# Performance work log

Measured on AMD Instinct MI355X. Metric: run time of the kernel, lower is better.

## Reference

```python
import jax, jax.numpy as jnp
import numpy as np

EPS = 1e-8

def setup_inputs() -> dict:
    key = jax.random.key(0)
    k1, k2, k3, k4, k5 = jax.random.split(key, 5)
    B, S, d, H = 4, 1024, 512, 8
    hd = d // H
    x = jax.random.normal(k1, (B, S, d), dtype=jnp.float32)
    V = jax.random.normal(k2, (B, S, H, hd), dtype=jnp.float32)
    # binary biological mask [B, S, S]
    M = (jax.random.uniform(k3, (B, S, S)) > 0.5).astype(jnp.float32)
    in_proj_w = jax.random.normal(k4, (3 * d, d), dtype=jnp.float32) * 0.02
    in_proj_b = jnp.zeros((3 * d,), dtype=jnp.float32)
    out_w = jax.random.normal(k5, (d, d), dtype=jnp.float32) * 0.02
    out_b = jnp.zeros((d,), dtype=jnp.float32)
    return {"x": x, "V": V, "M": M, "in_proj_w": in_proj_w,
            "in_proj_b": in_proj_b, "out_w": out_w, "out_b": out_b}


def reference(x, V, M, in_proj_w, in_proj_b, out_w, out_b):
    B, S, d = x.shape
    H, hd = V.shape[2], V.shape[3]
    # packed QKV projection (torch MHA in_proj); V slice is computed by torch
    # but its result is discarded, so only Q,K slices influence the output.
    qkv = x @ in_proj_w.T + in_proj_b            # [B, S, 3d]
    q = qkv[..., :d].reshape(B, S, H, hd).transpose(0, 2, 1, 3)        # [B,H,S,hd]
    k = qkv[..., d:2 * d].reshape(B, S, H, hd).transpose(0, 2, 1, 3)   # [B,H,S,hd]
    scores = jnp.einsum("bhqd,bhkd->bhqk", q, k) / jnp.sqrt(jnp.float32(hd))
    A = jax.nn.softmax(scores, axis=-1)           # [B,H,S,S] per-head attn weights
    # biological mask + L1 renormalization (post-hoc, as in original)
    A_sparse = A * M[:, None, :, :]
    norm = jnp.sum(jnp.abs(A_sparse), axis=-1, keepdims=True) + EPS
    A_bar = A_sparse / norm
    # custom V: [B,S,H,hd] -> [B,H,S,hd]
    Vp = V.transpose(0, 2, 1, 3)
    out = jnp.einsum("bhqk,bhkd->bhqd", A_bar, Vp)  # [B,H,S,hd]
    out = out.transpose(0, 2, 1, 3).reshape(B, S, d)
    return out @ out_w.T + out_b
```

## Files before the change

kernel.cpp:

```cpp
#include <hip/hip_runtime.h>
#include <hip/hip_bf16.h>

#define BB 4
#define SS 1024
#define DD 512
#define HH 8
#define HD 64

typedef __attribute__((ext_vector_type(8))) short bf16x8;
typedef __attribute__((ext_vector_type(4))) float f32x4;

static __device__ __forceinline__ unsigned short f2b(float f) {
  union { float f; unsigned int u; } c; c.f = f;
  return (unsigned short)((c.u + 0x7fffu + ((c.u >> 16) & 1u)) >> 16);
}

__global__ __launch_bounds__(256) void prep(
    const float* __restrict__ x, const float* __restrict__ W1,
    const float* __restrict__ Wo, const float* __restrict__ Mmask,
    const float* __restrict__ V, unsigned short* __restrict__ xb,
    unsigned short* __restrict__ W1b, unsigned short* __restrict__ Wob,
    unsigned char* __restrict__ Mpack, unsigned short* __restrict__ Vt) {
  __shared__ float Ls[64][65];
  const int bid = blockIdx.x;
  const int tid = threadIdx.x;

  if (bid < 1408) {
    const float* src; unsigned short* dst; size_t off;
    if (bid < 1024) { src = x;  dst = xb;  off = ((size_t)bid * 256 + tid) * 8; }
    else if (bid < 1280) { src = W1; dst = W1b; off = ((size_t)(bid - 1024) * 256 + tid) * 8; }
    else { src = Wo; dst = Wob; off = ((size_t)(bid - 1280) * 256 + tid) * 8; }
    const float4 a = *(const float4*)(src + off);
    const float4 b = *(const float4*)(src + off + 4);
    union { unsigned short s[8]; uint4 v; } o;
    o.s[0] = f2b(a.x); o.s[1] = f2b(a.y); o.s[2] = f2b(a.z); o.s[3] = f2b(a.w);
    o.s[4] = f2b(b.x); o.s[5] = f2b(b.y); o.s[6] = f2b(b.z); o.s[7] = f2b(b.w);
    *(uint4*)(dst + off) = o.v;
  } else if (bid < 3456) {
    const size_t g = (size_t)(bid - 1408) * 256 + tid;
    const float4 a = *(const float4*)(Mmask + g * 8);
    const float4 b = *(const float4*)(Mmask + g * 8 + 4);
    unsigned v = 0;
    v |= (a.x > 0.5f) ? 1u : 0u;   v |= (a.y > 0.5f) ? 2u : 0u;
    v |= (a.z > 0.5f) ? 4u : 0u;   v |= (a.w > 0.5f) ? 8u : 0u;
    v |= (b.x > 0.5f) ? 16u : 0u;  v |= (b.y > 0.5f) ? 32u : 0u;
    v |= (b.z > 0.5f) ? 64u : 0u;  v |= (b.w > 0.5f) ? 128u : 0u;
    Mpack[g] = (unsigned char)v;
  } else {
    const int id = bid - 3456;
    const int s0 = (id & 15) * 64, h = (id >> 4) & 7, b = id >> 7;
    {
      const int r = tid >> 2, cs = (tid & 3) * 16;
      const float* src = V + ((size_t)((b * SS + s0 + r) * HH) + h) * HD + cs;
#pragma unroll
      for (int j = 0; j < 4; j++) {
        const float4 v = *(const float4*)(src + j * 4);
        Ls[r][cs + j * 4 + 0] = v.x; Ls[r][cs + j * 4 + 1] = v.y;
        Ls[r][cs + j * 4 + 2] = v.z; Ls[r][cs + j * 4 + 3] = v.w;
      }
    }
    __syncthreads();
    {
      const int d = tid >> 2, ss = (tid & 3) * 16;
      union { unsigned short s[16]; uint4 v[2]; } o;
#pragma unroll
      for (int j = 0; j < 16; j++) o.s[j] = f2b(Ls[ss + j][d]);
      unsigned short* dst =
          Vt + ((size_t)((b * HH + h) * HD + d)) * SS + s0 + ss;
      *(uint4*)dst = o.v[0];
      *(uint4*)(dst + 8) = o.v[1];
    }
  }
}

__global__ __launch_bounds__(256) void gemm_qk(
    const unsigned short* __restrict__ xb, const unsigned short* __restrict__ W1b,
    const float* __restrict__ bias, unsigned short* __restrict__ qkb) {
  __shared__ unsigned short As[128][40];
  __shared__ unsigned short Bs[64][40];
  const int tid = threadIdx.x;
  const int lane = tid & 63, wave = tid >> 6;
  const int l16 = lane & 15, quad = lane >> 4;
  const int row0 = blockIdx.y * 128, col0 = blockIdx.x * 64;

  f32x4 acc[2][4];
#pragma unroll
  for (int i = 0; i < 2; i++)
#pragma unroll
    for (int j = 0; j < 4; j++) acc[i][j] = (f32x4){0.f, 0.f, 0.f, 0.f};

  for (int k0 = 0; k0 < DD; k0 += 32) {
    __syncthreads();
    {
      const int r = tid >> 1, cs = (tid & 1) * 16;
      const unsigned short* s = xb + (size_t)(row0 + r) * DD + k0 + cs;
      *(uint4*)&As[r][cs] = *(const uint4*)s;
      *(uint4*)&As[r][cs + 8] = *(const uint4*)(s + 8);
    }
    {
      const int r = tid >> 2, cs = (tid & 3) * 8;
      *(uint4*)&Bs[r][cs] =
          *(const uint4*)(W1b + (size_t)(col0 + r) * DD + k0 + cs);
    }
    __syncthreads();

    const bf16x8 a0 = *(const bf16x8*)&As[wave * 32 + l16][quad * 8];
    const bf16x8 a1 = *(const bf16x8*)&As[wave * 32 + 16 + l16][quad * 8];
#pragma unroll
    for (int nt = 0; nt < 4; nt++) {
      const bf16x8 bb = *(const bf16x8*)&Bs[nt * 16 + l16][quad * 8];
      acc[0][nt] = __builtin_amdgcn_mfma_f32_16x16x32_bf16(a0, bb, acc[0][nt], 0, 0, 0);
      acc[1][nt] = __builtin_amdgcn_mfma_f32_16x16x32_bf16(a1, bb, acc[1][nt], 0, 0, 0);
    }
  }

#pragma unroll
  for (int nt = 0; nt < 4; nt++) {
    const int col = col0 + nt * 16 + l16;
    const float bv = bias[col];
#pragma unroll
    for (int mi = 0; mi < 2; mi++)
#pragma unroll
      for (int reg = 0; reg < 4; reg++) {
        const int row = row0 + wave * 32 + mi * 16 + quad * 4 + reg;
        qkb[(size_t)row * 1024 + col] = f2b(acc[mi][nt][reg] + bv);
      }
  }
}

__global__ __launch_bounds__(256) void gemm_out(
    const unsigned short* __restrict__ Ab, const unsigned short* __restrict__ Wob,
    const float* __restrict__ bias, float* __restrict__ out) {
  __shared__ unsigned short As[64][40];
  __shared__ unsigned short Bs[64][40];
  const int tid = threadIdx.x;
  const int lane = tid & 63, wave = tid >> 6;
  const int l16 = lane & 15, quad = lane >> 4;
  const int row0 = blockIdx.y * 64, col0 = blockIdx.x * 64;

  f32x4 acc[4];
#pragma unroll
  for (int j = 0; j < 4; j++) acc[j] = (f32x4){0.f, 0.f, 0.f, 0.f};

  for (int k0 = 0; k0 < DD; k0 += 32) {
    __syncthreads();
    {
      const int r = tid >> 2, cs = (tid & 3) * 8;
      *(uint4*)&As[r][cs] =
          *(const uint4*)(Ab + (size_t)(row0 + r) * DD + k0 + cs);
      *(uint4*)&Bs[r][cs] =
          *(const uint4*)(Wob + (size_t)(col0 + r) * DD + k0 + cs);
    }
    __syncthreads();

    const bf16x8 a0 = *(const bf16x8*)&As[wave * 16 + l16][quad * 8];
#pragma unroll
    for (int nt = 0; nt < 4; nt++) {
      const bf16x8 bb = *(const bf16x8*)&Bs[nt * 16 + l16][quad * 8];
      acc[nt] = __builtin_amdgcn_mfma_f32_16x16x32_bf16(a0, bb, acc[nt], 0, 0, 0);
    }
  }

#pragma unroll
  for (int nt = 0; nt < 4; nt++) {
    const int col = col0 + nt * 16 + l16;
    const float bv = bias[col];
#pragma unroll
    for (int reg = 0; reg < 4; reg++) {
      const int row = row0 + wave * 16 + quad * 4 + reg;
      out[(size_t)row * DD + col] = acc[nt][reg] + bv;
    }
  }
}

__global__ __launch_bounds__(256) void flash_attn_split(
    const unsigned short* __restrict__ qkb, const unsigned short* __restrict__ Vt,
    const unsigned char* __restrict__ Mpack, float* __restrict__ Opart,
    float* __restrict__ Sms) {
  __shared__ unsigned short QP[64][72];
  __shared__ unsigned short Ks[64][72];
  __shared__ unsigned short Vs[64][72];

  const int tid = threadIdx.x;
  const int lane = tid & 63, wave = tid >> 6;
  const int l16 = lane & 15, quad = lane >> 4;
  const int q0 = blockIdx.x * 64;
  const int h = blockIdx.y & 7, sp = blockIdx.y >> 3;
  const int b = blockIdx.z;

  {
    const int r = tid >> 2, cs = (tid & 3) * 16;
    const unsigned short* s = qkb + (size_t)(b * SS + q0 + r) * 1024 + h * HD + cs;
    *(uint4*)&QP[r][cs] = *(const uint4*)s;
    *(uint4*)&QP[r][cs + 8] = *(const uint4*)(s + 8);
  }

  union { uint4 v[4]; unsigned w[16]; } mu;
  {
    const uint4* mp = (const uint4*)(Mpack +
        (size_t)(b * SS + q0 + wave * 16 + l16) * 128 + sp * 64);
    mu.v[0] = mp[0]; mu.v[1] = mp[1]; mu.v[2] = mp[2]; mu.v[3] = mp[3];
  }

  __syncthreads();
  const bf16x8 bQ0 = *(const bf16x8*)&QP[wave * 16 + l16][quad * 8];
  const bf16x8 bQ1 = *(const bf16x8*)&QP[wave * 16 + l16][32 + quad * 8];
  unsigned short(*Ps)[72] = (unsigned short(*)[72]) & QP[wave * 16][0];

  float Smp = 0.f;
  f32x4 O[4];
#pragma unroll
  for (int i = 0; i < 4; i++) O[i] = (f32x4){0.f, 0.f, 0.f, 0.f};

#pragma unroll
  for (int i = 0; i < 8; i++) {
    const int k0 = (sp * 8 + i) * 64;
    const unsigned mlo = mu.w[2 * i], mhi = mu.w[2 * i + 1];

    __syncthreads();
    {
      const int r = tid >> 2, cs = (tid & 3) * 16;
      const unsigned short* s =
          qkb + (size_t)(b * SS + k0 + r) * 1024 + DD + h * HD + cs;
      *(uint4*)&Ks[r][cs] = *(const uint4*)s;
      *(uint4*)&Ks[r][cs + 8] = *(const uint4*)(s + 8);
    }
    {
      const int d = tid >> 2, cs = (tid & 3) * 16;
      const unsigned short* s =
          Vt + ((size_t)((b * HH + h) * HD + d)) * SS + k0 + cs;
      *(uint4*)&Vs[d][cs] = *(const uint4*)s;
      *(uint4*)&Vs[d][cs + 8] = *(const uint4*)(s + 8);
    }
    __syncthreads();

#pragma unroll
    for (int t = 0; t < 4; t++) {
      const bf16x8 aK0 = *(const bf16x8*)&Ks[t * 16 + l16][quad * 8];
      const bf16x8 aK1 = *(const bf16x8*)&Ks[t * 16 + l16][32 + quad * 8];
      f32x4 a = (f32x4){0.f, 0.f, 0.f, 0.f};
      a = __builtin_amdgcn_mfma_f32_16x16x32_bf16(aK0, bQ0, a, 0, 0, 0);
      a = __builtin_amdgcn_mfma_f32_16x16x32_bf16(aK1, bQ1, a, 0, 0, 0);
      const unsigned nib =
          ((t < 2 ? mlo : mhi) >> ((t & 1) * 16 + quad * 4)) & 0xFu;
      float e0 = __expf(a[0] * 0.125f); e0 = (nib & 1u) ? e0 : 0.f;
      float e1 = __expf(a[1] * 0.125f); e1 = (nib & 2u) ? e1 : 0.f;
      float e2 = __expf(a[2] * 0.125f); e2 = (nib & 4u) ? e2 : 0.f;
      float e3 = __expf(a[3] * 0.125f); e3 = (nib & 8u) ? e3 : 0.f;
      Smp += (e0 + e1) + (e2 + e3);
      uint2 w;
      w.x = (unsigned)f2b(e0) | ((unsigned)f2b(e1) << 16);
      w.y = (unsigned)f2b(e2) | ((unsigned)f2b(e3) << 16);
      *(uint2*)&Ps[l16][t * 16 + quad * 4] = w;
    }

    const bf16x8 aP0 = *(const bf16x8*)&Ps[l16][quad * 8];
    const bf16x8 aP1 = *(const bf16x8*)&Ps[l16][32 + quad * 8];
#pragma unroll
    for (int dt = 0; dt < 4; dt++) {
      const bf16x8 bV0 = *(const bf16x8*)&Vs[dt * 16 + l16][quad * 8];
      const bf16x8 bV1 = *(const bf16x8*)&Vs[dt * 16 + l16][32 + quad * 8];
      O[dt] = __builtin_amdgcn_mfma_f32_16x16x32_bf16(aP0, bV0, O[dt], 0, 0, 0);
      O[dt] = __builtin_amdgcn_mfma_f32_16x16x32_bf16(aP1, bV1, O[dt], 0, 0, 0);
    }
  }

  Smp += __shfl_xor(Smp, 16);
  Smp += __shfl_xor(Smp, 32);
  const size_t grow0 = (size_t)(b * HH + h) * SS + q0 + wave * 16;
  const int NR = BB * HH * SS;
  if (lane < 16) Sms[(size_t)sp * NR + grow0 + lane] = Smp;
#pragma unroll
  for (int reg = 0; reg < 4; reg++) {
    const size_t obase = ((size_t)sp * NR + grow0 + quad * 4 + reg) * HD;
#pragma unroll
    for (int dt = 0; dt < 4; dt++)
      Opart[obase + dt * 16 + l16] = O[dt][reg];
  }
}

__global__ __launch_bounds__(256) void combine(
    const float* __restrict__ Opart, const float* __restrict__ Sms,
    unsigned short* __restrict__ attnb) {
  const int idx = blockIdx.x * 256 + threadIdx.x;
  const int row = idx >> 4;
  const int d = (idx & 15) * 4;
  const int NR = BB * HH * SS;
  const float4 o0 = *(const float4*)(Opart + (size_t)row * HD + d);
  const float4 o1 = *(const float4*)(Opart + ((size_t)NR + row) * HD + d);
  const float s = Sms[row] + Sms[NR + row];
  const float inv = 1.0f / (s + 1e-12f);
  const int b = row >> 13, h = (row >> 10) & 7, q = row & 1023;
  union { unsigned short us[4]; uint2 v; } o;
  o.us[0] = f2b((o0.x + o1.x) * inv);
  o.us[1] = f2b((o0.y + o1.y) * inv);
  o.us[2] = f2b((o0.z + o1.z) * inv);
  o.us[3] = f2b((o0.w + o1.w) * inv);
  *(uint2*)(attnb + (size_t)(b * SS + q) * DD + h * HD + d) = o.v;
}

extern "C" void kernel_launch(void* const* d_in, const int* in_sizes, int n_in,
                              void* d_out, int out_size, void* d_ws,
                              size_t ws_size, hipStream_t stream) {
  const float* x = (const float*)d_in[0];
  const float* V = (const float*)d_in[1];
  const float* Mmask = (const float*)d_in[2];
  const float* in_proj_w = (const float*)d_in[3];
  const float* in_proj_b = (const float*)d_in[4];
  const float* out_w = (const float*)d_in[5];
  const float* out_b = (const float*)d_in[6];
  float* out = (float*)d_out;

  unsigned char* ws = (unsigned char*)d_ws;
  unsigned short* qkb   = (unsigned short*)(ws);
  unsigned short* xb    = (unsigned short*)(ws + (8ull << 20));
  unsigned short* W1b   = (unsigned short*)(ws + (12ull << 20));
  unsigned short* Wob   = (unsigned short*)(ws + (13ull << 20));
  unsigned short* Vt    = (unsigned short*)(ws + (14ull << 20));
  unsigned short* attnb = (unsigned short*)(ws + (18ull << 20));
  float*          Opart = (float*)(ws + (22ull << 20));
  float*          Sms   = (float*)(ws + (38ull << 20));
  unsigned char*  Mpack = ws + (38ull << 20) + (256u << 10);

  prep<<<3968, 256, 0, stream>>>(x, in_proj_w, out_w, Mmask, V,
                                 xb, W1b, Wob, Mpack, Vt);
  gemm_qk<<<dim3(16, 32), 256, 0, stream>>>(xb, W1b, in_proj_b, qkb);
  flash_attn_split<<<dim3(SS / 64, 2 * HH, BB), 256, 0, stream>>>(
      qkb, Vt, Mpack, Opart, Sms);
  combine<<<2048, 256, 0, stream>>>(Opart, Sms, attnb);
  gemm_out<<<dim3(8, 64), 256, 0, stream>>>(attnb, Wob, out_b, out);
}
```

Measured before the change: 144.2 us.

## Fuse split-K attention combine into a 512-thread attention block via LDS reduction

The attention kernel now runs both key halves inside one 512-thread block. Waves 4-7 handle the second half of the keys and pass their partial outputs and row sums through shared memory, so the block writes normalized bf16 output directly. This removes the separate combine kernel and the fp32 partial-output round trip through global memory. Separately, the QK projection GEMM tile shrinks from 128 to 64 rows, doubling its grid. The larger block and added shared memory may lower attention occupancy, and the smaller GEMM tile reduces reuse of the loaded weight tile.

```diff
diff --git a/kernel.cpp b/kernel.cpp
--- a/kernel.cpp
+++ b/kernel.cpp
@@ -76,41 +76,33 @@
 __global__ __launch_bounds__(256) void gemm_qk(
     const unsigned short* __restrict__ xb, const unsigned short* __restrict__ W1b,
     const float* __restrict__ bias, unsigned short* __restrict__ qkb) {
-  __shared__ unsigned short As[128][40];
+  __shared__ unsigned short As[64][40];
   __shared__ unsigned short Bs[64][40];
   const int tid = threadIdx.x;
   const int lane = tid & 63, wave = tid >> 6;
   const int l16 = lane & 15, quad = lane >> 4;
-  const int row0 = blockIdx.y * 128, col0 = blockIdx.x * 64;
-
-  f32x4 acc[2][4];
-#pragma unroll
-  for (int i = 0; i < 2; i++)
-#pragma unroll
-    for (int j = 0; j < 4; j++) acc[i][j] = (f32x4){0.f, 0.f, 0.f, 0.f};
+  const int row0 = blockIdx.y * 64, col0 = blockIdx.x * 64;
+
+  f32x4 acc[4];
+#pragma unroll
+  for (int j = 0; j < 4; j++) acc[j] = (f32x4){0.f, 0.f, 0.f, 0.f};
 
   for (int k0 = 0; k0 < DD; k0 += 32) {
     __syncthreads();
     {
-      const int r = tid >> 1, cs = (tid & 1) * 16;
-      const unsigned short* s = xb + (size_t)(row0 + r) * DD + k0 + cs;
-      *(uint4*)&As[r][cs] = *(const uint4*)s;
-      *(uint4*)&As[r][cs + 8] = *(const uint4*)(s + 8);
-    }
-    {
       const int r = tid >> 2, cs = (tid & 3) * 8;
+      *(uint4*)&As[r][cs] =
+          *(const uint4*)(xb + (size_t)(row0 + r) * DD + k0 + cs);
       *(uint4*)&Bs[r][cs] =
           *(const uint4*)(W1b + (size_t)(col0 + r) * DD + k0 + cs);
     }
     __syncthreads();
 
-    const bf16x8 a0 = *(const bf16x8*)&As[wave * 32 + l16][quad * 8];
-    const bf16x8 a1 = *(const bf16x8*)&As[wave * 32 + 16 + l16][quad * 8];
+    const bf16x8 a0 = *(const bf16x8*)&As[wave * 16 + l16][quad * 8];
 #pragma unroll
     for (int nt = 0; nt < 4; nt++) {
       const bf16x8 bb = *(const bf16x8*)&Bs[nt * 16 + l16][quad * 8];
-      acc[0][nt] = __builtin_amdgcn_mfma_f32_16x16x32_bf16(a0, bb, acc[0][nt], 0, 0, 0);
-      acc[1][nt] = __builtin_amdgcn_mfma_f32_16x16x32_bf16(a1, bb, acc[1][nt], 0, 0, 0);
+      acc[nt] = __builtin_amdgcn_mfma_f32_16x16x32_bf16(a0, bb, acc[nt], 0, 0, 0);
     }
   }
 
@@ -119,12 +111,10 @@
     const int col = col0 + nt * 16 + l16;
     const float bv = bias[col];
 #pragma unroll
-    for (int mi = 0; mi < 2; mi++)
-#pragma unroll
-      for (int reg = 0; reg < 4; reg++) {
-        const int row = row0 + wave * 32 + mi * 16 + quad * 4 + reg;
-        qkb[(size_t)row * 1024 + col] = f2b(acc[mi][nt][reg] + bv);
-      }
+    for (int reg = 0; reg < 4; reg++) {
+      const int row = row0 + wave * 16 + quad * 4 + reg;
+      qkb[(size_t)row * 1024 + col] = f2b(acc[nt][reg] + bv);
+    }
   }
 }
 
@@ -173,71 +163,69 @@
   }
 }
 
-__global__ __launch_bounds__(256) void flash_attn_split(
+__global__ __launch_bounds__(512) void flash_attn(
     const unsigned short* __restrict__ qkb, const unsigned short* __restrict__ Vt,
-    const unsigned char* __restrict__ Mpack, float* __restrict__ Opart,
-    float* __restrict__ Sms) {
-  __shared__ unsigned short QP[64][72];
-  __shared__ unsigned short Ks[64][72];
-  __shared__ unsigned short Vs[64][72];
+    const unsigned char* __restrict__ Mpack, unsigned short* __restrict__ attnb) {
+  __shared__ unsigned short Qs[64][72];
+  __shared__ unsigned short Ks[2][64][72];
+  __shared__ unsigned short Vs[2][64][72];
+  __shared__ unsigned short Ps[8][16][72];
 
   const int tid = threadIdx.x;
   const int lane = tid & 63, wave = tid >> 6;
   const int l16 = lane & 15, quad = lane >> 4;
+  const int qg = wave & 3, kh = wave >> 2;
   const int q0 = blockIdx.x * 64;
-  const int h = blockIdx.y & 7, sp = blockIdx.y >> 3;
+  const int h = blockIdx.y;
   const int b = blockIdx.z;
 
   {
-    const int r = tid >> 2, cs = (tid & 3) * 16;
-    const unsigned short* s = qkb + (size_t)(b * SS + q0 + r) * 1024 + h * HD + cs;
-    *(uint4*)&QP[r][cs] = *(const uint4*)s;
-    *(uint4*)&QP[r][cs + 8] = *(const uint4*)(s + 8);
+    const int r = tid >> 3, cs = (tid & 7) * 8;
+    *(uint4*)&Qs[r][cs] =
+        *(const uint4*)(qkb + (size_t)(b * SS + q0 + r) * 1024 + h * HD + cs);
   }
 
   union { uint4 v[4]; unsigned w[16]; } mu;
   {
     const uint4* mp = (const uint4*)(Mpack +
-        (size_t)(b * SS + q0 + wave * 16 + l16) * 128 + sp * 64);
+        (size_t)(b * SS + q0 + qg * 16 + l16) * 128 + kh * 64);
     mu.v[0] = mp[0]; mu.v[1] = mp[1]; mu.v[2] = mp[2]; mu.v[3] = mp[3];
   }
 
   __syncthreads();
-  const bf16x8 bQ0 = *(const bf16x8*)&QP[wave * 16 + l16][quad * 8];
-  const bf16x8 bQ1 = *(const bf16x8*)&QP[wave * 16 + l16][32 + quad * 8];
-  unsigned short(*Ps)[72] = (unsigned short(*)[72]) & QP[wave * 16][0];
+  const bf16x8 bQ0 = *(const bf16x8*)&Qs[qg * 16 + l16][quad * 8];
+  const bf16x8 bQ1 = *(const bf16x8*)&Qs[qg * 16 + l16][32 + quad * 8];
 
   float Smp = 0.f;
   f32x4 O[4];
 #pragma unroll
   for (int i = 0; i < 4; i++) O[i] = (f32x4){0.f, 0.f, 0.f, 0.f};
 
-#pragma unroll
+  const unsigned short* kbase = qkb + (size_t)(b * SS) * 1024 + DD + h * HD;
+  const unsigned short* vbase = Vt + (size_t)((b * HH + h) * HD) * SS;
+
+#pragma unroll 2
   for (int i = 0; i < 8; i++) {
-    const int k0 = (sp * 8 + i) * 64;
     const unsigned mlo = mu.w[2 * i], mhi = mu.w[2 * i + 1];
 
     __syncthreads();
     {
-      const int r = tid >> 2, cs = (tid & 3) * 16;
-      const unsigned short* s =
-          qkb + (size_t)(b * SS + k0 + r) * 1024 + DD + h * HD + cs;
-      *(uint4*)&Ks[r][cs] = *(const uint4*)s;
-      *(uint4*)&Ks[r][cs + 8] = *(const uint4*)(s + 8);
-    }
-    {
-      const int d = tid >> 2, cs = (tid & 3) * 16;
-      const unsigned short* s =
-          Vt + ((size_t)((b * HH + h) * HD + d)) * SS + k0 + cs;
-      *(uint4*)&Vs[d][cs] = *(const uint4*)s;
-      *(uint4*)&Vs[d][cs + 8] = *(const uint4*)(s + 8);
+      const int r = tid >> 3, cs = (tid & 7) * 8;
+      *(uint4*)&Ks[0][r][cs] =
+          *(const uint4*)(kbase + (size_t)(i * 64 + r) * 1024 + cs);
+      *(uint4*)&Ks[1][r][cs] =
+          *(const uint4*)(kbase + (size_t)(512 + i * 64 + r) * 1024 + cs);
+      *(uint4*)&Vs[0][r][cs] =
+          *(const uint4*)(vbase + (size_t)r * SS + i * 64 + cs);
+      *(uint4*)&Vs[1][r][cs] =
+          *(const uint4*)(vbase + (size_t)r * SS + 512 + i * 64 + cs);
     }
     __syncthreads();
 
 #pragma unroll
     for (int t = 0; t < 4; t++) {
-      const bf16x8 aK0 = *(const bf16x8*)&Ks[t * 16 + l16][quad * 8];
-      const bf16x8 aK1 = *(const bf16x8*)&Ks[t * 16 + l16][32 + quad * 8];
+      const bf16x8 aK0 = *(const bf16x8*)&Ks[kh][t * 16 + l16][quad * 8];
+      const bf16x8 aK1 = *(const bf16x8*)&Ks[kh][t * 16 + l16][32 + quad * 8];
       f32x4 a = (f32x4){0.f, 0.f, 0.f, 0.f};
       a = __builtin_amdgcn_mfma_f32_16x16x32_bf16(aK0, bQ0, a, 0, 0, 0);
       a = __builtin_amdgcn_mfma_f32_16x16x32_bf16(aK1, bQ1, a, 0, 0, 0);
@@ -251,15 +239,15 @@
       uint2 w;
       w.x = (unsigned)f2b(e0) | ((unsigned)f2b(e1) << 16);
       w.y = (unsigned)f2b(e2) | ((unsigned)f2b(e3) << 16);
-      *(uint2*)&Ps[l16][t * 16 + quad * 4] = w;
-    }
-
-    const bf16x8 aP0 = *(const bf16x8*)&Ps[l16][quad * 8];
-    const bf16x8 aP1 = *(const bf16x8*)&Ps[l16][32 + quad * 8];
+      *(uint2*)&Ps[wave][l16][t * 16 + quad * 4] = w;
+    }
+
+    const bf16x8 aP0 = *(const bf16x8*)&Ps[wave][l16][quad * 8];
+    const bf16x8 aP1 = *(const bf16x8*)&Ps[wave][l16][32 + quad * 8];
 #pragma unroll
     for (int dt = 0; dt < 4; dt++) {
-      const bf16x8 bV0 = *(const bf16x8*)&Vs[dt * 16 + l16][quad * 8];
-      const bf16x8 bV1 = *(const bf16x8*)&Vs[dt * 16 + l16][32 + quad * 8];
+      const bf16x8 bV0 = *(const bf16x8*)&Vs[kh][dt * 16 + l16][quad * 8];
+      const bf16x8 bV1 = *(const bf16x8*)&Vs[kh][dt * 16 + l16][32 + quad * 8];
       O[dt] = __builtin_amdgcn_mfma_f32_16x16x32_bf16(aP0, bV0, O[dt], 0, 0, 0);
       O[dt] = __builtin_amdgcn_mfma_f32_16x16x32_bf16(aP1, bV1, O[dt], 0, 0, 0);
     }
@@ -267,36 +255,42 @@
 
   Smp += __shfl_xor(Smp, 16);
   Smp += __shfl_xor(Smp, 32);
-  const size_t grow0 = (size_t)(b * HH + h) * SS + q0 + wave * 16;
-  const int NR = BB * HH * SS;
-  if (lane < 16) Sms[(size_t)sp * NR + grow0 + lane] = Smp;
-#pragma unroll
-  for (int reg = 0; reg < 4; reg++) {
-    const size_t obase = ((size_t)sp * NR + grow0 + quad * 4 + reg) * HD;
-#pragma unroll
-    for (int dt = 0; dt < 4; dt++)
-      Opart[obase + dt * 16 + l16] = O[dt][reg];
-  }
-}
-
-__global__ __launch_bounds__(256) void combine(
-    const float* __restrict__ Opart, const float* __restrict__ Sms,
-    unsigned short* __restrict__ attnb) {
-  const int idx = blockIdx.x * 256 + threadIdx.x;
-  const int row = idx >> 4;
-  const int d = (idx & 15) * 4;
-  const int NR = BB * HH * SS;
-  const float4 o0 = *(const float4*)(Opart + (size_t)row * HD + d);
-  const float4 o1 = *(const float4*)(Opart + ((size_t)NR + row) * HD + d);
-  const float s = Sms[row] + Sms[NR + row];
-  const float inv = 1.0f / (s + 1e-12f);
-  const int b = row >> 13, h = (row >> 10) & 7, q = row & 1023;
-  union { unsigned short us[4]; uint2 v; } o;
-  o.us[0] = f2b((o0.x + o1.x) * inv);
-  o.us[1] = f2b((o0.y + o1.y) * inv);
-  o.us[2] = f2b((o0.z + o1.z) * inv);
-  o.us[3] = f2b((o0.w + o1.w) * inv);
-  *(uint2*)(attnb + (size_t)(b * SS + q) * DD + h * HD + d) = o.v;
+
+  __syncthreads();
+  float* scratch = (float*)&Ps[0][0][0];
+  float* Obuf = scratch;
+  float* SmT = scratch + 4096;
+
+  if (lane < 16) SmT[kh * 64 + qg * 16 + lane] = Smp;
+  if (kh == 1) {
+#pragma unroll
+    for (int reg = 0; reg < 4; reg++)
+#pragma unroll
+      for (int dt = 0; dt < 4; dt++)
+        Obuf[qg * 1024 + (quad * 4 + reg) * 64 + dt * 16 + l16] = O[dt][reg];
+  }
+  __syncthreads();
+
+  if (kh == 0) {
+    float invr[4];
+#pragma unroll
+    for (int reg = 0; reg < 4; reg++) {
+      const int qi = qg * 16 + quad * 4 + reg;
+      const float s = SmT[qi] + SmT[64 + qi];
+      invr[reg] = 1.0f / (s + 1e-12f);
+    }
+#pragma unroll
+    for (int reg = 0; reg < 4; reg++) {
+      const size_t row = (size_t)(b * SS + q0 + qg * 16 + quad * 4 + reg);
+#pragma unroll
+      for (int dt = 0; dt < 4; dt++) {
+        const float o =
+            (O[dt][reg] + Obuf[qg * 1024 + (quad * 4 + reg) * 64 + dt * 16 + l16]) *
+            invr[reg];
+        attnb[row * DD + h * HD + dt * 16 + l16] = f2b(o);
+      }
+    }
+  }
 }
 
 extern "C" void kernel_launch(void* const* d_in, const int* in_sizes, int n_in,
@@ -318,15 +312,11 @@
   unsigned short* Wob   = (unsigned short*)(ws + (13ull << 20));
   unsigned short* Vt    = (unsigned short*)(ws + (14ull << 20));
   unsigned short* attnb = (unsigned short*)(ws + (18ull << 20));
-  float*          Opart = (float*)(ws + (22ull << 20));
-  float*          Sms   = (float*)(ws + (38ull << 20));
-  unsigned char*  Mpack = ws + (38ull << 20) + (256u << 10);
+  unsigned char*  Mpack = ws + (22ull << 20);
 
   prep<<<3968, 256, 0, stream>>>(x, in_proj_w, out_w, Mmask, V,
                                  xb, W1b, Wob, Mpack, Vt);
-  gemm_qk<<<dim3(16, 32), 256, 0, stream>>>(xb, W1b, in_proj_b, qkb);
-  flash_attn_split<<<dim3(SS / 64, 2 * HH, BB), 256, 0, stream>>>(
-      qkb, Vt, Mpack, Opart, Sms);
-  combine<<<2048, 256, 0, stream>>>(Opart, Sms, attnb);
+  gemm_qk<<<dim3(16, 64), 256, 0, stream>>>(xb, W1b, in_proj_b, qkb);
+  flash_attn<<<dim3(SS / 64, HH, BB), 512, 0, stream>>>(qkb, Vt, Mpack, attnb);
   gemm_out<<<dim3(8, 64), 256, 0, stream>>>(attnb, Wob, out_b, out);
 }
```

Result: no change. 146.7 us (+1.7%).

## Fuse split attention and combine; widen GEMM K-tiles and fold Q scale

Applied to the files above, without the earlier changes.

The two-way key-split attention kernel and its separate combine kernel are replaced by one attention kernel per (query tile, head, batch). It loops over all 16 key tiles and normalizes by the row sum before writing bf16 output directly. This removes the fp32 partial-output round trip through global memory and one kernel launch, but halves the number of attention blocks. Both GEMMs now stage 64-wide K tiles, and gemm_out uses 128-row tiles, which halves barrier count and improves operand reuse. The 1/sqrt(hd) scale is folded into Q in the projection epilogue, removing a multiply per score.

```diff
diff --git a/kernel.cpp b/kernel.cpp
--- a/kernel.cpp
+++ b/kernel.cpp
@@ -76,8 +76,8 @@
 __global__ __launch_bounds__(256) void gemm_qk(
     const unsigned short* __restrict__ xb, const unsigned short* __restrict__ W1b,
     const float* __restrict__ bias, unsigned short* __restrict__ qkb) {
-  __shared__ unsigned short As[128][40];
-  __shared__ unsigned short Bs[64][40];
+  __shared__ unsigned short As[128][72];
+  __shared__ unsigned short Bs[64][72];
   const int tid = threadIdx.x;
   const int lane = tid & 63, wave = tid >> 6;
   const int l16 = lane & 15, quad = lane >> 4;
@@ -89,28 +89,33 @@
 #pragma unroll
     for (int j = 0; j < 4; j++) acc[i][j] = (f32x4){0.f, 0.f, 0.f, 0.f};
 
-  for (int k0 = 0; k0 < DD; k0 += 32) {
-    __syncthreads();
-    {
-      const int r = tid >> 1, cs = (tid & 1) * 16;
+  for (int k0 = 0; k0 < DD; k0 += 64) {
+    __syncthreads();
+    {
+      const int r = tid >> 1, cs = (tid & 1) * 32;
       const unsigned short* s = xb + (size_t)(row0 + r) * DD + k0 + cs;
-      *(uint4*)&As[r][cs] = *(const uint4*)s;
-      *(uint4*)&As[r][cs + 8] = *(const uint4*)(s + 8);
-    }
-    {
-      const int r = tid >> 2, cs = (tid & 3) * 8;
-      *(uint4*)&Bs[r][cs] =
-          *(const uint4*)(W1b + (size_t)(col0 + r) * DD + k0 + cs);
-    }
-    __syncthreads();
-
-    const bf16x8 a0 = *(const bf16x8*)&As[wave * 32 + l16][quad * 8];
-    const bf16x8 a1 = *(const bf16x8*)&As[wave * 32 + 16 + l16][quad * 8];
-#pragma unroll
-    for (int nt = 0; nt < 4; nt++) {
-      const bf16x8 bb = *(const bf16x8*)&Bs[nt * 16 + l16][quad * 8];
-      acc[0][nt] = __builtin_amdgcn_mfma_f32_16x16x32_bf16(a0, bb, acc[0][nt], 0, 0, 0);
-      acc[1][nt] = __builtin_amdgcn_mfma_f32_16x16x32_bf16(a1, bb, acc[1][nt], 0, 0, 0);
+#pragma unroll
+      for (int j = 0; j < 4; j++)
+        *(uint4*)&As[r][cs + j * 8] = *(const uint4*)(s + j * 8);
+    }
+    {
+      const int r = tid >> 2, cs = (tid & 3) * 16;
+      const unsigned short* s = W1b + (size_t)(col0 + r) * DD + k0 + cs;
+      *(uint4*)&Bs[r][cs] = *(const uint4*)s;
+      *(uint4*)&Bs[r][cs + 8] = *(const uint4*)(s + 8);
+    }
+    __syncthreads();
+
+#pragma unroll
+    for (int kk = 0; kk < 64; kk += 32) {
+      const bf16x8 a0 = *(const bf16x8*)&As[wave * 32 + l16][kk + quad * 8];
+      const bf16x8 a1 = *(const bf16x8*)&As[wave * 32 + 16 + l16][kk + quad * 8];
+#pragma unroll
+      for (int nt = 0; nt < 4; nt++) {
+        const bf16x8 bb = *(const bf16x8*)&Bs[nt * 16 + l16][kk + quad * 8];
+        acc[0][nt] = __builtin_amdgcn_mfma_f32_16x16x32_bf16(a0, bb, acc[0][nt], 0, 0, 0);
+        acc[1][nt] = __builtin_amdgcn_mfma_f32_16x16x32_bf16(a1, bb, acc[1][nt], 0, 0, 0);
+      }
     }
   }
 
@@ -118,12 +123,13 @@
   for (int nt = 0; nt < 4; nt++) {
     const int col = col0 + nt * 16 + l16;
     const float bv = bias[col];
+    const float scale = (col < DD) ? 0.125f : 1.0f;
 #pragma unroll
     for (int mi = 0; mi < 2; mi++)
 #pragma unroll
       for (int reg = 0; reg < 4; reg++) {
         const int row = row0 + wave * 32 + mi * 16 + quad * 4 + reg;
-        qkb[(size_t)row * 1024 + col] = f2b(acc[mi][nt][reg] + bv);
+        qkb[(size_t)row * 1024 + col] = f2b((acc[mi][nt][reg] + bv) * scale);
       }
   }
 }
@@ -131,33 +137,46 @@
 __global__ __launch_bounds__(256) void gemm_out(
     const unsigned short* __restrict__ Ab, const unsigned short* __restrict__ Wob,
     const float* __restrict__ bias, float* __restrict__ out) {
-  __shared__ unsigned short As[64][40];
-  __shared__ unsigned short Bs[64][40];
+  __shared__ unsigned short As[128][72];
+  __shared__ unsigned short Bs[64][72];
   const int tid = threadIdx.x;
   const int lane = tid & 63, wave = tid >> 6;
   const int l16 = lane & 15, quad = lane >> 4;
-  const int row0 = blockIdx.y * 64, col0 = blockIdx.x * 64;
-
-  f32x4 acc[4];
-#pragma unroll
-  for (int j = 0; j < 4; j++) acc[j] = (f32x4){0.f, 0.f, 0.f, 0.f};
-
-  for (int k0 = 0; k0 < DD; k0 += 32) {
-    __syncthreads();
-    {
-      const int r = tid >> 2, cs = (tid & 3) * 8;
-      *(uint4*)&As[r][cs] =
-          *(const uint4*)(Ab + (size_t)(row0 + r) * DD + k0 + cs);
-      *(uint4*)&Bs[r][cs] =
-          *(const uint4*)(Wob + (size_t)(col0 + r) * DD + k0 + cs);
-    }
-    __syncthreads();
-
-    const bf16x8 a0 = *(const bf16x8*)&As[wave * 16 + l16][quad * 8];
-#pragma unroll
-    for (int nt = 0; nt < 4; nt++) {
-      const bf16x8 bb = *(const bf16x8*)&Bs[nt * 16 + l16][quad * 8];
-      acc[nt] = __builtin_amdgcn_mfma_f32_16x16x32_bf16(a0, bb, acc[nt], 0, 0, 0);
+  const int row0 = blockIdx.y * 128, col0 = blockIdx.x * 64;
+
+  f32x4 acc[2][4];
+#pragma unroll
+  for (int i = 0; i < 2; i++)
+#pragma unroll
+    for (int j = 0; j < 4; j++) acc[i][j] = (f32x4){0.f, 0.f, 0.f, 0.f};
+
+  for (int k0 = 0; k0 < DD; k0 += 64) {
+    __syncthreads();
+    {
+      const int r = tid >> 1, cs = (tid & 1) * 32;
+      const unsigned short* s = Ab + (size_t)(row0 + r) * DD + k0 + cs;
+#pragma unroll
+      for (int j = 0; j < 4; j++)
+        *(uint4*)&As[r][cs + j * 8] = *(const uint4*)(s + j * 8);
+    }
+    {
+      const int r = tid >> 2, cs = (tid & 3) * 16;
+      const unsigned short* s = Wob + (size_t)(col0 + r) * DD + k0 + cs;
+      *(uint4*)&Bs[r][cs] = *(const uint4*)s;
+      *(uint4*)&Bs[r][cs + 8] = *(const uint4*)(s + 8);
+    }
+    __syncthreads();
+
+#pragma unroll
+    for (int kk = 0; kk < 64; kk += 32) {
+      const bf16x8 a0 = *(const bf16x8*)&As[wave * 32 + l16][kk + quad * 8];
+      const bf16x8 a1 = *(const bf16x8*)&As[wave * 32 + 16 + l16][kk + quad * 8];
+#pragma unroll
+      for (int nt = 0; nt < 4; nt++) {
+        const bf16x8 bb = *(const bf16x8*)&Bs[nt * 16 + l16][kk + quad * 8];
+        acc[0][nt] = __builtin_amdgcn_mfma_f32_16x16x32_bf16(a0, bb, acc[0][nt], 0, 0, 0);
+        acc[1][nt] = __builtin_amdgcn_mfma_f32_16x16x32_bf16(a1, bb, acc[1][nt], 0, 0, 0);
+      }
     }
   }
 
@@ -166,71 +185,64 @@
     const int col = col0 + nt * 16 + l16;
     const float bv = bias[col];
 #pragma unroll
-    for (int reg = 0; reg < 4; reg++) {
-      const int row = row0 + wave * 16 + quad * 4 + reg;
-      out[(size_t)row * DD + col] = acc[nt][reg] + bv;
-    }
-  }
-}
-
-__global__ __launch_bounds__(256) void flash_attn_split(
+    for (int mi = 0; mi < 2; mi++)
+#pragma unroll
+      for (int reg = 0; reg < 4; reg++) {
+        const int row = row0 + wave * 32 + mi * 16 + quad * 4 + reg;
+        out[(size_t)row * DD + col] = acc[mi][nt][reg] + bv;
+      }
+  }
+}
+
+__global__ __launch_bounds__(256) void flash_attn(
     const unsigned short* __restrict__ qkb, const unsigned short* __restrict__ Vt,
-    const unsigned char* __restrict__ Mpack, float* __restrict__ Opart,
-    float* __restrict__ Sms) {
-  __shared__ unsigned short QP[64][72];
+    const unsigned char* __restrict__ Mpack, unsigned short* __restrict__ attnb) {
+  __shared__ unsigned short Qs[64][72];
   __shared__ unsigned short Ks[64][72];
   __shared__ unsigned short Vs[64][72];
+  __shared__ unsigned short Ps[4][16][72];
+  __shared__ float SmT[4][16];
 
   const int tid = threadIdx.x;
   const int lane = tid & 63, wave = tid >> 6;
   const int l16 = lane & 15, quad = lane >> 4;
   const int q0 = blockIdx.x * 64;
-  const int h = blockIdx.y & 7, sp = blockIdx.y >> 3;
+  const int h = blockIdx.y;
   const int b = blockIdx.z;
 
   {
     const int r = tid >> 2, cs = (tid & 3) * 16;
     const unsigned short* s = qkb + (size_t)(b * SS + q0 + r) * 1024 + h * HD + cs;
-    *(uint4*)&QP[r][cs] = *(const uint4*)s;
-    *(uint4*)&QP[r][cs + 8] = *(const uint4*)(s + 8);
-  }
-
-  union { uint4 v[4]; unsigned w[16]; } mu;
-  {
-    const uint4* mp = (const uint4*)(Mpack +
-        (size_t)(b * SS + q0 + wave * 16 + l16) * 128 + sp * 64);
-    mu.v[0] = mp[0]; mu.v[1] = mp[1]; mu.v[2] = mp[2]; mu.v[3] = mp[3];
-  }
-
-  __syncthreads();
-  const bf16x8 bQ0 = *(const bf16x8*)&QP[wave * 16 + l16][quad * 8];
-  const bf16x8 bQ1 = *(const bf16x8*)&QP[wave * 16 + l16][32 + quad * 8];
-  unsigned short(*Ps)[72] = (unsigned short(*)[72]) & QP[wave * 16][0];
+    *(uint4*)&Qs[r][cs] = *(const uint4*)s;
+    *(uint4*)&Qs[r][cs + 8] = *(const uint4*)(s + 8);
+  }
+  const bf16x8 bQ0 = *(const bf16x8*)&Qs[wave * 16 + l16][quad * 8];
+  const bf16x8 bQ1 = *(const bf16x8*)&Qs[wave * 16 + l16][32 + quad * 8];
+
+  const unsigned char* mrowp =
+      Mpack + (size_t)(b * SS + q0 + wave * 16 + l16) * 128;
 
   float Smp = 0.f;
   f32x4 O[4];
 #pragma unroll
   for (int i = 0; i < 4; i++) O[i] = (f32x4){0.f, 0.f, 0.f, 0.f};
 
-#pragma unroll
-  for (int i = 0; i < 8; i++) {
-    const int k0 = (sp * 8 + i) * 64;
-    const unsigned mlo = mu.w[2 * i], mhi = mu.w[2 * i + 1];
+  const unsigned short* kbase = qkb + (size_t)(b * SS) * 1024 + DD + h * HD;
+  const unsigned short* vbase = Vt + (size_t)((b * HH + h) * HD) * SS;
+
+#pragma unroll 2
+  for (int i = 0; i < 16; i++) {
+    const uint2 mm = *(const uint2*)(mrowp + i * 8);
 
     __syncthreads();
     {
       const int r = tid >> 2, cs = (tid & 3) * 16;
-      const unsigned short* s =
-          qkb + (size_t)(b * SS + k0 + r) * 1024 + DD + h * HD + cs;
+      const unsigned short* s = kbase + (size_t)(i * 64 + r) * 1024 + cs;
       *(uint4*)&Ks[r][cs] = *(const uint4*)s;
       *(uint4*)&Ks[r][cs + 8] = *(const uint4*)(s + 8);
-    }
-    {
-      const int d = tid >> 2, cs = (tid & 3) * 16;
-      const unsigned short* s =
-          Vt + ((size_t)((b * HH + h) * HD + d)) * SS + k0 + cs;
-      *(uint4*)&Vs[d][cs] = *(const uint4*)s;
-      *(uint4*)&Vs[d][cs + 8] = *(const uint4*)(s + 8);
+      const unsigned short* v = vbase + (size_t)r * SS + i * 64 + cs;
+      *(uint4*)&Vs[r][cs] = *(const uint4*)v;
+      *(uint4*)&Vs[r][cs + 8] = *(const uint4*)(v + 8);
     }
     __syncthreads();
 
@@ -242,20 +254,20 @@
       a = __builtin_amdgcn_mfma_f32_16x16x32_bf16(aK0, bQ0, a, 0, 0, 0);
       a = __builtin_amdgcn_mfma_f32_16x16x32_bf16(aK1, bQ1, a, 0, 0, 0);
       const unsigned nib =
-          ((t < 2 ? mlo : mhi) >> ((t & 1) * 16 + quad * 4)) & 0xFu;
-      float e0 = __expf(a[0] * 0.125f); e0 = (nib & 1u) ? e0 : 0.f;
-      float e1 = __expf(a[1] * 0.125f); e1 = (nib & 2u) ? e1 : 0.f;
-      float e2 = __expf(a[2] * 0.125f); e2 = (nib & 4u) ? e2 : 0.f;
-      float e3 = __expf(a[3] * 0.125f); e3 = (nib & 8u) ? e3 : 0.f;
+          ((t < 2 ? mm.x : mm.y) >> ((t & 1) * 16 + quad * 4)) & 0xFu;
+      float e0 = __expf(a[0]); e0 = (nib & 1u) ? e0 : 0.f;
+      float e1 = __expf(a[1]); e1 = (nib & 2u) ? e1 : 0.f;
+      float e2 = __expf(a[2]); e2 = (nib & 4u) ? e2 : 0.f;
+      float e3 = __expf(a[3]); e3 = (nib & 8u) ? e3 : 0.f;
       Smp += (e0 + e1) + (e2 + e3);
       uint2 w;
       w.x = (unsigned)f2b(e0) | ((unsigned)f2b(e1) << 16);
       w.y = (unsigned)f2b(e2) | ((unsigned)f2b(e3) << 16);
-      *(uint2*)&Ps[l16][t * 16 + quad * 4] = w;
-    }
-
-    const bf16x8 aP0 = *(const bf16x8*)&Ps[l16][quad * 8];
-    const bf16x8 aP1 = *(const bf16x8*)&Ps[l16][32 + quad * 8];
+      *(uint2*)&Ps[wave][l16][t * 16 + quad * 4] = w;
+    }
+
+    const bf16x8 aP0 = *(const bf16x8*)&Ps[wave][l16][quad * 8];
+    const bf16x8 aP1 = *(const bf16x8*)&Ps[wave][l16][32 + quad * 8];
 #pragma unroll
     for (int dt = 0; dt < 4; dt++) {
       const bf16x8 bV0 = *(const bf16x8*)&Vs[dt * 16 + l16][quad * 8];
@@ -267,36 +279,18 @@
 
   Smp += __shfl_xor(Smp, 16);
   Smp += __shfl_xor(Smp, 32);
-  const size_t grow0 = (size_t)(b * HH + h) * SS + q0 + wave * 16;
-  const int NR = BB * HH * SS;
-  if (lane < 16) Sms[(size_t)sp * NR + grow0 + lane] = Smp;
+  if (lane < 16) SmT[wave][lane] = Smp;
+  float invr[4];
+#pragma unroll
+  for (int reg = 0; reg < 4; reg++)
+    invr[reg] = 1.0f / (SmT[wave][quad * 4 + reg] + 1e-12f);
 #pragma unroll
   for (int reg = 0; reg < 4; reg++) {
-    const size_t obase = ((size_t)sp * NR + grow0 + quad * 4 + reg) * HD;
+    const size_t row = (size_t)(b * SS + q0 + wave * 16 + quad * 4 + reg);
 #pragma unroll
     for (int dt = 0; dt < 4; dt++)
-      Opart[obase + dt * 16 + l16] = O[dt][reg];
-  }
-}
-
-__global__ __launch_bounds__(256) void combine(
-    const float* __restrict__ Opart, const float* __restrict__ Sms,
-    unsigned short* __restrict__ attnb) {
-  const int idx = blockIdx.x * 256 + threadIdx.x;
-  const int row = idx >> 4;
-  const int d = (idx & 15) * 4;
-  const int NR = BB * HH * SS;
-  const float4 o0 = *(const float4*)(Opart + (size_t)row * HD + d);
-  const float4 o1 = *(const float4*)(Opart + ((size_t)NR + row) * HD + d);
-  const float s = Sms[row] + Sms[NR + row];
-  const float inv = 1.0f / (s + 1e-12f);
-  const int b = row >> 13, h = (row >> 10) & 7, q = row & 1023;
-  union { unsigned short us[4]; uint2 v; } o;
-  o.us[0] = f2b((o0.x + o1.x) * inv);
-  o.us[1] = f2b((o0.y + o1.y) * inv);
-  o.us[2] = f2b((o0.z + o1.z) * inv);
-  o.us[3] = f2b((o0.w + o1.w) * inv);
-  *(uint2*)(attnb + (size_t)(b * SS + q) * DD + h * HD + d) = o.v;
+      attnb[row * DD + h * HD + dt * 16 + l16] = f2b(O[dt][reg] * invr[reg]);
+  }
 }
 
 extern "C" void kernel_launch(void* const* d_in, const int* in_sizes, int n_in,
@@ -318,15 +312,11 @@
   unsigned short* Wob   = (unsigned short*)(ws + (13ull << 20));
   unsigned short* Vt    = (unsigned short*)(ws + (14ull << 20));
   unsigned short* attnb = (unsigned short*)(ws + (18ull << 20));
-  float*          Opart = (float*)(ws + (22ull << 20));
-  float*          Sms   = (float*)(ws + (38ull << 20));
-  unsigned char*  Mpack = ws + (38ull << 20) + (256u << 10);
+  unsigned char*  Mpack = ws + (22ull << 20);
 
   prep<<<3968, 256, 0, stream>>>(x, in_proj_w, out_w, Mmask, V,
                                  xb, W1b, Wob, Mpack, Vt);
   gemm_qk<<<dim3(16, 32), 256, 0, stream>>>(xb, W1b, in_proj_b, qkb);
-  flash_attn_split<<<dim3(SS / 64, 2 * HH, BB), 256, 0, stream>>>(
-      qkb, Vt, Mpack, Opart, Sms);
-  combine<<<2048, 256, 0, stream>>>(Opart, Sms, attnb);
-  gemm_out<<<dim3(8, 64), 256, 0, stream>>>(attnb, Wob, out_b, out);
-}
+  flash_attn<<<dim3(SS / 64, HH, BB), 256, 0, stream>>>(qkb, Vt, Mpack, attnb);
+  gemm_out<<<dim3(8, 32), 256, 0, stream>>>(attnb, Wob, out_b, out);
+}
```

New measurement: 149.6 us. 3.7% more time.

## Fuse x bf16 conversion into QK GEMM, load A directly, fold softmax scale

Applied to the files above, without the earlier changes.

Drops the separate fp32-to-bf16 conversion of x in the prep kernel. gemm_qk now reads x in fp32 straight from global memory into registers and converts it there. Both GEMMs stop staging the A operand in shared memory and double the K step to 64. The 1/sqrt(hd) scale is folded into the Q columns at the GEMM epilogue, so the attention kernel no longer multiplies scores before exp. This saves a full write and reread of x, but the A loads are now uncoalesced per-lane global reads with no reuse across waves.

```diff
diff --git a/kernel.cpp b/kernel.cpp
--- a/kernel.cpp
+++ b/kernel.cpp
@@ -15,29 +15,36 @@
   return (unsigned short)((c.u + 0x7fffu + ((c.u >> 16) & 1u)) >> 16);
 }
 
+static __device__ __forceinline__ bf16x8 ld_cvt8(const float* p) {
+  const float4 f0 = *(const float4*)p;
+  const float4 f1 = *(const float4*)(p + 4);
+  union { unsigned short s[8]; bf16x8 v; } o;
+  o.s[0] = f2b(f0.x); o.s[1] = f2b(f0.y); o.s[2] = f2b(f0.z); o.s[3] = f2b(f0.w);
+  o.s[4] = f2b(f1.x); o.s[5] = f2b(f1.y); o.s[6] = f2b(f1.z); o.s[7] = f2b(f1.w);
+  return o.v;
+}
+
 __global__ __launch_bounds__(256) void prep(
-    const float* __restrict__ x, const float* __restrict__ W1,
-    const float* __restrict__ Wo, const float* __restrict__ Mmask,
-    const float* __restrict__ V, unsigned short* __restrict__ xb,
+    const float* __restrict__ W1, const float* __restrict__ Wo,
+    const float* __restrict__ Mmask, const float* __restrict__ V,
     unsigned short* __restrict__ W1b, unsigned short* __restrict__ Wob,
     unsigned char* __restrict__ Mpack, unsigned short* __restrict__ Vt) {
   __shared__ float Ls[64][65];
   const int bid = blockIdx.x;
   const int tid = threadIdx.x;
 
-  if (bid < 1408) {
+  if (bid < 384) {
     const float* src; unsigned short* dst; size_t off;
-    if (bid < 1024) { src = x;  dst = xb;  off = ((size_t)bid * 256 + tid) * 8; }
-    else if (bid < 1280) { src = W1; dst = W1b; off = ((size_t)(bid - 1024) * 256 + tid) * 8; }
-    else { src = Wo; dst = Wob; off = ((size_t)(bid - 1280) * 256 + tid) * 8; }
+    if (bid < 256) { src = W1; dst = W1b; off = ((size_t)bid * 256 + tid) * 8; }
+    else { src = Wo; dst = Wob; off = ((size_t)(bid - 256) * 256 + tid) * 8; }
     const float4 a = *(const float4*)(src + off);
     const float4 b = *(const float4*)(src + off + 4);
     union { unsigned short s[8]; uint4 v; } o;
     o.s[0] = f2b(a.x); o.s[1] = f2b(a.y); o.s[2] = f2b(a.z); o.s[3] = f2b(a.w);
     o.s[4] = f2b(b.x); o.s[5] = f2b(b.y); o.s[6] = f2b(b.z); o.s[7] = f2b(b.w);
     *(uint4*)(dst + off) = o.v;
-  } else if (bid < 3456) {
-    const size_t g = (size_t)(bid - 1408) * 256 + tid;
+  } else if (bid < 2432) {
+    const size_t g = (size_t)(bid - 384) * 256 + tid;
     const float4 a = *(const float4*)(Mmask + g * 8);
     const float4 b = *(const float4*)(Mmask + g * 8 + 4);
     unsigned v = 0;
@@ -47,7 +54,7 @@
     v |= (b.z > 0.5f) ? 64u : 0u;  v |= (b.w > 0.5f) ? 128u : 0u;
     Mpack[g] = (unsigned char)v;
   } else {
-    const int id = bid - 3456;
+    const int id = bid - 2432;
     const int s0 = (id & 15) * 64, h = (id >> 4) & 7, b = id >> 7;
     {
       const int r = tid >> 2, cs = (tid & 3) * 16;
@@ -74,10 +81,9 @@
 }
 
 __global__ __launch_bounds__(256) void gemm_qk(
-    const unsigned short* __restrict__ xb, const unsigned short* __restrict__ W1b,
+    const float* __restrict__ x, const unsigned short* __restrict__ W1b,
     const float* __restrict__ bias, unsigned short* __restrict__ qkb) {
-  __shared__ unsigned short As[128][40];
-  __shared__ unsigned short Bs[64][40];
+  __shared__ unsigned short Bs[64][72];
   const int tid = threadIdx.x;
   const int lane = tid & 63, wave = tid >> 6;
   const int l16 = lane & 15, quad = lane >> 4;
@@ -89,28 +95,29 @@
 #pragma unroll
     for (int j = 0; j < 4; j++) acc[i][j] = (f32x4){0.f, 0.f, 0.f, 0.f};
 
-  for (int k0 = 0; k0 < DD; k0 += 32) {
-    __syncthreads();
-    {
-      const int r = tid >> 1, cs = (tid & 1) * 16;
-      const unsigned short* s = xb + (size_t)(row0 + r) * DD + k0 + cs;
-      *(uint4*)&As[r][cs] = *(const uint4*)s;
-      *(uint4*)&As[r][cs + 8] = *(const uint4*)(s + 8);
-    }
-    {
-      const int r = tid >> 2, cs = (tid & 3) * 8;
-      *(uint4*)&Bs[r][cs] =
-          *(const uint4*)(W1b + (size_t)(col0 + r) * DD + k0 + cs);
-    }
-    __syncthreads();
-
-    const bf16x8 a0 = *(const bf16x8*)&As[wave * 32 + l16][quad * 8];
-    const bf16x8 a1 = *(const bf16x8*)&As[wave * 32 + 16 + l16][quad * 8];
-#pragma unroll
-    for (int nt = 0; nt < 4; nt++) {
-      const bf16x8 bb = *(const bf16x8*)&Bs[nt * 16 + l16][quad * 8];
-      acc[0][nt] = __builtin_amdgcn_mfma_f32_16x16x32_bf16(a0, bb, acc[0][nt], 0, 0, 0);
-      acc[1][nt] = __builtin_amdgcn_mfma_f32_16x16x32_bf16(a1, bb, acc[1][nt], 0, 0, 0);
+  const float* arow0 = x + (size_t)(row0 + wave * 32 + l16) * DD + quad * 8;
+  const float* arow1 = arow0 + (size_t)16 * DD;
+
+  for (int k0 = 0; k0 < DD; k0 += 64) {
+    __syncthreads();
+    {
+      const int r = tid >> 2, cs = (tid & 3) * 16;
+      const unsigned short* s = W1b + (size_t)(col0 + r) * DD + k0 + cs;
+      *(uint4*)&Bs[r][cs] = *(const uint4*)s;
+      *(uint4*)&Bs[r][cs + 8] = *(const uint4*)(s + 8);
+    }
+    __syncthreads();
+
+#pragma unroll
+    for (int kk = 0; kk < 64; kk += 32) {
+      const bf16x8 a0 = ld_cvt8(arow0 + k0 + kk);
+      const bf16x8 a1 = ld_cvt8(arow1 + k0 + kk);
+#pragma unroll
+      for (int nt = 0; nt < 4; nt++) {
+        const bf16x8 bb = *(const bf16x8*)&Bs[nt * 16 + l16][kk + quad * 8];
+        acc[0][nt] = __builtin_amdgcn_mfma_f32_16x16x32_bf16(a0, bb, acc[0][nt], 0, 0, 0);
+        acc[1][nt] = __builtin_amdgcn_mfma_f32_16x16x32_bf16(a1, bb, acc[1][nt], 0, 0, 0);
+      }
     }
   }
 
@@ -118,12 +125,13 @@
   for (int nt = 0; nt < 4; nt++) {
     const int col = col0 + nt * 16 + l16;
     const float bv = bias[col];
+    const float scale = (col < DD) ? 0.125f : 1.0f;
 #pragma unroll
     for (int mi = 0; mi < 2; mi++)
 #pragma unroll
       for (int reg = 0; reg < 4; reg++) {
         const int row = row0 + wave * 32 + mi * 16 + quad * 4 + reg;
-        qkb[(size_t)row * 1024 + col] = f2b(acc[mi][nt][reg] + bv);
+        qkb[(size_t)row * 1024 + col] = f2b((acc[mi][nt][reg] + bv) * scale);
       }
   }
 }
@@ -131,8 +139,7 @@
 __global__ __launch_bounds__(256) void gemm_out(
     const unsigned short* __restrict__ Ab, const unsigned short* __restrict__ Wob,
     const float* __restrict__ bias, float* __restrict__ out) {
-  __shared__ unsigned short As[64][40];
-  __shared__ unsigned short Bs[64][40];
+  __shared__ unsigned short Bs[64][72];
   const int tid = threadIdx.x;
   const int lane = tid & 63, wave = tid >> 6;
   const int l16 = lane & 15, quad = lane >> 4;
@@ -142,22 +149,27 @@
 #pragma unroll
   for (int j = 0; j < 4; j++) acc[j] = (f32x4){0.f, 0.f, 0.f, 0.f};
 
-  for (int k0 = 0; k0 < DD; k0 += 32) {
-    __syncthreads();
-    {
-      const int r = tid >> 2, cs = (tid & 3) * 8;
-      *(uint4*)&As[r][cs] =
-          *(const uint4*)(Ab + (size_t)(row0 + r) * DD + k0 + cs);
-      *(uint4*)&Bs[r][cs] =
-          *(const uint4*)(Wob + (size_t)(col0 + r) * DD + k0 + cs);
-    }
-    __syncthreads();
-
-    const bf16x8 a0 = *(const bf16x8*)&As[wave * 16 + l16][quad * 8];
-#pragma unroll
-    for (int nt = 0; nt < 4; nt++) {
-      const bf16x8 bb = *(const bf16x8*)&Bs[nt * 16 + l16][quad * 8];
-      acc[nt] = __builtin_amdgcn_mfma_f32_16x16x32_bf16(a0, bb, acc[nt], 0, 0, 0);
+  const unsigned short* arow =
+      Ab + (size_t)(row0 + wave * 16 + l16) * DD + quad * 8;
+
+  for (int k0 = 0; k0 < DD; k0 += 64) {
+    __syncthreads();
+    {
+      const int r = tid >> 2, cs = (tid & 3) * 16;
+      const unsigned short* s = Wob + (size_t)(col0 + r) * DD + k0 + cs;
+      *(uint4*)&Bs[r][cs] = *(const uint4*)s;
+      *(uint4*)&Bs[r][cs + 8] = *(const uint4*)(s + 8);
+    }
+    __syncthreads();
+
+#pragma unroll
+    for (int kk = 0; kk < 64; kk += 32) {
+      const bf16x8 a0 = *(const bf16x8*)(arow + k0 + kk);
+#pragma unroll
+      for (int nt = 0; nt < 4; nt++) {
+        const bf16x8 bb = *(const bf16x8*)&Bs[nt * 16 + l16][kk + quad * 8];
+        acc[nt] = __builtin_amdgcn_mfma_f32_16x16x32_bf16(a0, bb, acc[nt], 0, 0, 0);
+      }
     }
   }
 
@@ -243,10 +255,10 @@
       a = __builtin_amdgcn_mfma_f32_16x16x32_bf16(aK1, bQ1, a, 0, 0, 0);
       const unsigned nib =
           ((t < 2 ? mlo : mhi) >> ((t & 1) * 16 + quad * 4)) & 0xFu;
-      float e0 = __expf(a[0] * 0.125f); e0 = (nib & 1u) ? e0 : 0.f;
-      float e1 = __expf(a[1] * 0.125f); e1 = (nib & 2u) ? e1 : 0.f;
-      float e2 = __expf(a[2] * 0.125f); e2 = (nib & 4u) ? e2 : 0.f;
-      float e3 = __expf(a[3] * 0.125f); e3 = (nib & 8u) ? e3 : 0.f;
+      float e0 = __expf(a[0]); e0 = (nib & 1u) ? e0 : 0.f;
+      float e1 = __expf(a[1]); e1 = (nib & 2u) ? e1 : 0.f;
+      float e2 = __expf(a[2]); e2 = (nib & 4u) ? e2 : 0.f;
+      float e3 = __expf(a[3]); e3 = (nib & 8u) ? e3 : 0.f;
       Smp += (e0 + e1) + (e2 + e3);
       uint2 w;
       w.x = (unsigned)f2b(e0) | ((unsigned)f2b(e1) << 16);
@@ -313,18 +325,17 @@
 
   unsigned char* ws = (unsigned char*)d_ws;
   unsigned short* qkb   = (unsigned short*)(ws);
-  unsigned short* xb    = (unsigned short*)(ws + (8ull << 20));
-  unsigned short* W1b   = (unsigned short*)(ws + (12ull << 20));
-  unsigned short* Wob   = (unsigned short*)(ws + (13ull << 20));
-  unsigned short* Vt    = (unsigned short*)(ws + (14ull << 20));
-  unsigned short* attnb = (unsigned short*)(ws + (18ull << 20));
-  float*          Opart = (float*)(ws + (22ull << 20));
-  float*          Sms   = (float*)(ws + (38ull << 20));
-  unsigned char*  Mpack = ws + (38ull << 20) + (256u << 10);
-
-  prep<<<3968, 256, 0, stream>>>(x, in_proj_w, out_w, Mmask, V,
-                                 xb, W1b, Wob, Mpack, Vt);
-  gemm_qk<<<dim3(16, 32), 256, 0, stream>>>(xb, W1b, in_proj_b, qkb);
+  unsigned short* W1b   = (unsigned short*)(ws + (8ull << 20));
+  unsigned short* Wob   = (unsigned short*)(ws + (9ull << 20));
+  unsigned short* Vt    = (unsigned short*)(ws + (10ull << 20));
+  unsigned short* attnb = (unsigned short*)(ws + (14ull << 20));
+  float*          Opart = (float*)(ws + (18ull << 20));
+  float*          Sms   = (float*)(ws + (34ull << 20));
+  unsigned char*  Mpack = ws + (34ull << 20) + (256u << 10);
+
+  prep<<<2944, 256, 0, stream>>>(in_proj_w, out_w, Mmask, V,
+                                 W1b, Wob, Mpack, Vt);
+  gemm_qk<<<dim3(16, 32), 256, 0, stream>>>(x, W1b, in_proj_b, qkb);
   flash_attn_split<<<dim3(SS / 64, 2 * HH, BB), 256, 0, stream>>>(
       qkb, Vt, Mpack, Opart, Sms);
   combine<<<2048, 256, 0, stream>>>(Opart, Sms, attnb);
```

Result: slower. 163.1 us (+13.1%).
